# Performance work log

Measured on AMD Instinct MI355X. Metric: run time of the kernel, lower is better.

## Reference

```python
import jax, jax.numpy as jnp
import numpy as np

N_NODES = 100000
N_EDGES = 3200000
DIM = 64


def setup_inputs() -> dict:
    key = jax.random.key(0)
    k1, k2, k3, k4, k5, k6 = jax.random.split(key, 6)
    lap_rows = jax.random.randint(k1, (N_EDGES,), 0, N_NODES, dtype=jnp.int32)
    lap_cols = jax.random.randint(k2, (N_EDGES,), 0, N_NODES, dtype=jnp.int32)
    # normalized-Laplacian-like positive values
    lap_vals = jax.random.uniform(k3, (N_EDGES,), dtype=jnp.float32) * 0.1
    features = jax.random.normal(k4, (N_NODES, DIM), dtype=jnp.float32)
    scale = 1.0 / np.sqrt(DIM)
    W1 = jax.random.normal(k5, (DIM, DIM), dtype=jnp.float32) * scale
    b1 = jnp.zeros((DIM,), dtype=jnp.float32)
    W2 = jax.random.normal(k6, (DIM, DIM), dtype=jnp.float32) * scale
    b2 = jnp.zeros((DIM,), dtype=jnp.float32)
    return {
        "lap_rows": lap_rows, "lap_cols": lap_cols, "lap_vals": lap_vals,
        "features": features, "W1": W1, "b1": b1, "W2": W2, "b2": b2,
    }


def reference(lap_rows, lap_cols, lap_vals, features, W1, b1, W2, b2):
    # x = L @ features  (COO SpMM: gather source rows, scale, scatter-add to dest)
    msgs = lap_vals[:, None] * features[lap_cols]            # [E, D]
    x = jax.ops.segment_sum(msgs, lap_rows, num_segments=N_NODES)  # [N, D]
    # output = (L+I) E W1 + (L E * E) W2
    inter_part1 = (features + x) @ W1 + b1                   # [N, D_out]
    inter_part2 = (x * features) @ W2 + b2                   # [N, D_out]
    return inter_part1 + inter_part2
```

## Files before the change

### kernel.cpp

```cpp
#include <hip/hip_runtime.h>
#include <hip/hip_fp16.h>

#define DIM 64
#define RPB 64
#define RPB_SHIFT 6
#define CAP 6144
#define CAPK (CAP / 1024)
#define HTILE 16384

typedef _Float16 half8 __attribute__((ext_vector_type(8)));
typedef float    f32x4 __attribute__((ext_vector_type(4)));

__global__ __launch_bounds__(256) void scatter_kernel(
    const int* __restrict__ rows, const int* __restrict__ cols,
    const float* __restrict__ vals, const float* __restrict__ feat,
    float* __restrict__ x, int E)
{
    unsigned long long t = (unsigned long long)blockIdx.x * blockDim.x + threadIdx.x;
    int e = (int)(t >> 6);
    int d = (int)(t & 63);
    if (e >= E) return;
    int r = rows[e];
    int c = cols[e];
    float v = vals[e];
    float f = feat[(size_t)c * DIM + d];
    atomicAdd(&x[(size_t)r * DIM + d], v * f);
}

__global__ __launch_bounds__(256) void cvt_kernel(
    const float* __restrict__ f, __half* __restrict__ h, int n2)
{
    int i = blockIdx.x * blockDim.x + threadIdx.x;
    if (i < n2) {
        float2 v = ((const float2*)f)[i];
        __half2 o;
        o.x = __float2half(v.x);
        o.y = __float2half(v.y);
        ((__half2*)h)[i] = o;
    }
}

__global__ __launch_bounds__(1024) void hist_kernel(
    const int* __restrict__ rows, int* __restrict__ gcnt, int E, int B)
{
    extern __shared__ int lcnt[];
    for (int i = threadIdx.x; i < B; i += 1024) lcnt[i] = 0;
    __syncthreads();
    int base = blockIdx.x * HTILE;
#pragma unroll
    for (int k = 0; k < HTILE / 1024; ++k) {
        int e = base + k * 1024 + threadIdx.x;
        if (e < E) atomicAdd(&lcnt[rows[e] >> RPB_SHIFT], 1);
    }
    __syncthreads();
    for (int i = threadIdx.x; i < B; i += 1024)
        if (lcnt[i]) atomicAdd(&gcnt[i], lcnt[i]);
}

__global__ __launch_bounds__(1024) void scan_kernel(
    const int* __restrict__ gcnt, int* __restrict__ offs,
    int* __restrict__ cursors, int B, int E)
{
    __shared__ int lds[2048];
    int t = threadIdx.x;
    int c0 = (t < B) ? gcnt[t] : 0;
    int c1 = (t + 1024 < B) ? gcnt[t + 1024] : 0;
    lds[t] = c0;
    lds[t + 1024] = c1;
    __syncthreads();
    for (int off = 1; off < 2048; off <<= 1) {
        int a = (t >= off) ? lds[t - off] : 0;
        int b = lds[t + 1024 - off];
        __syncthreads();
        lds[t] += a;
        lds[t + 1024] += b;
        __syncthreads();
    }
    if (t < B)        { offs[t] = lds[t] - c0;               cursors[t] = lds[t] - c0; }
    if (t + 1024 < B) { offs[t + 1024] = lds[t + 1024] - c1; cursors[t + 1024] = lds[t + 1024] - c1; }
    if (t == 0) offs[B] = E;
}

__global__ __launch_bounds__(1024) void binpack_kernel(
    const int* __restrict__ rows, const int* __restrict__ cols,
    const float* __restrict__ vals, int* __restrict__ cursors,
    unsigned long long* __restrict__ sorted, int E, int B)
{
    extern __shared__ int l[];
    int* cnt = l;
    int* bse = l + B;
    for (int i = threadIdx.x; i < B; i += 1024) cnt[i] = 0;
    __syncthreads();
    int tbase = blockIdx.x * HTILE;
#pragma unroll
    for (int k = 0; k < HTILE / 1024; ++k) {
        int e = tbase + k * 1024 + threadIdx.x;
        if (e < E) atomicAdd(&cnt[rows[e] >> RPB_SHIFT], 1);
    }
    __syncthreads();
    for (int i = threadIdx.x; i < B; i += 1024) {
        int c = cnt[i];
        bse[i] = c ? atomicAdd(&cursors[i], c) : 0;
    }
    __syncthreads();
    for (int i = threadIdx.x; i < B; i += 1024) cnt[i] = 0;
    __syncthreads();
#pragma unroll
    for (int k = 0; k < HTILE / 1024; ++k) {
        int e = tbase + k * 1024 + threadIdx.x;
        if (e < E) {
            int r = rows[e];
            int b = r >> RPB_SHIFT;
            int slot = bse[b] + atomicAdd(&cnt[b], 1);
            unsigned long long pk =
                ((unsigned long long)__float_as_uint(vals[e]) << 32) |
                ((unsigned long long)(r & (RPB - 1)) << 17) |
                (unsigned)cols[e];
            sorted[slot] = pk;
        }
    }
}

__global__ __launch_bounds__(1024) void reduce_fused_kernel(
    const unsigned long long* __restrict__ sorted, const int* __restrict__ offs,
    const __half* __restrict__ featH, float* __restrict__ x, int N)
{
    __shared__ unsigned long long spk[CAP];
    __shared__ int rcnt[RPB];
    __shared__ int rbase[RPB];

    const int tid = threadIdx.x;
    const int b   = blockIdx.x;
    const int s    = offs[b];
    const int tend = offs[b + 1];
    int nl = tend - s;
    if (nl > CAP) nl = CAP;

    if (tid < RPB) rcnt[tid] = 0;
    __syncthreads();

    unsigned long long pkreg[CAPK];
#pragma unroll
    for (int k = 0; k < CAPK; ++k) {
        int i = k * 1024 + tid;
        pkreg[k] = (i < nl) ? sorted[s + i] : 0ull;
    }
#pragma unroll
    for (int k = 0; k < CAPK; ++k) {
        int i = k * 1024 + tid;
        if (i < nl) atomicAdd(&rcnt[(int)((pkreg[k] >> 17) & (RPB - 1))], 1);
    }
    __syncthreads();

    if (tid < 64) {
        int c = rcnt[tid];
        int v = c;
#pragma unroll
        for (int off = 1; off < 64; off <<= 1) {
            int u = __shfl_up(v, off, 64);
            if (tid >= off) v += u;
        }
        rbase[tid] = v - c;
        rcnt[tid]  = 0;
    }
    __syncthreads();

#pragma unroll
    for (int k = 0; k < CAPK; ++k) {
        int i = k * 1024 + tid;
        if (i < nl) {
            int rl  = (int)((pkreg[k] >> 17) & (RPB - 1));
            int idx = atomicAdd(&rcnt[rl], 1);
            spk[rbase[rl] + idx] = pkreg[k];
        }
    }
    __syncthreads();

    const int w    = tid >> 6;
    const int lane = tid & 63;
    const int eg   = lane >> 3;
    const int sub  = lane & 7;
    const int rowbase = b * RPB;

#pragma unroll
    for (int j = 0; j < RPB / 16; ++j) {
        int rl = w + 16 * j;
        int rs = rbase[rl];
        int rt = rs + rcnt[rl];

        __half2 hacc[4];
#pragma unroll
        for (int q = 0; q < 4; ++q) hacc[q] = __floats2half2_rn(0.f, 0.f);

        int i = rs + eg;
        for (; i + 24 < rt; i += 32) {
            unsigned long long pk0 = spk[i];
            unsigned long long pk1 = spk[i + 8];
            unsigned long long pk2 = spk[i + 16];
            unsigned long long pk3 = spk[i + 24];
            float4 rw0 = *(const float4*)(featH + (size_t)(pk0 & 0x1FFFFu) * DIM + sub * 8);
            float4 rw1 = *(const float4*)(featH + (size_t)(pk1 & 0x1FFFFu) * DIM + sub * 8);
            float4 rw2 = *(const float4*)(featH + (size_t)(pk2 & 0x1FFFFu) * DIM + sub * 8);
            float4 rw3 = *(const float4*)(featH + (size_t)(pk3 & 0x1FFFFu) * DIM + sub * 8);
            __half2 v0 = __float2half2_rn(__uint_as_float((unsigned)(pk0 >> 32)));
            __half2 v1 = __float2half2_rn(__uint_as_float((unsigned)(pk1 >> 32)));
            __half2 v2 = __float2half2_rn(__uint_as_float((unsigned)(pk2 >> 32)));
            __half2 v3 = __float2half2_rn(__uint_as_float((unsigned)(pk3 >> 32)));
            hacc[0] = __hfma2(v0, __builtin_bit_cast(__half2, rw0.x), hacc[0]);
            hacc[1] = __hfma2(v0, __builtin_bit_cast(__half2, rw0.y), hacc[1]);
            hacc[2] = __hfma2(v0, __builtin_bit_cast(__half2, rw0.z), hacc[2]);
            hacc[3] = __hfma2(v0, __builtin_bit_cast(__half2, rw0.w), hacc[3]);
            hacc[0] = __hfma2(v1, __builtin_bit_cast(__half2, rw1.x), hacc[0]);
            hacc[1] = __hfma2(v1, __builtin_bit_cast(__half2, rw1.y), hacc[1]);
            hacc[2] = __hfma2(v1, __builtin_bit_cast(__half2, rw1.z), hacc[2]);
            hacc[3] = __hfma2(v1, __builtin_bit_cast(__half2, rw1.w), hacc[3]);
            hacc[0] = __hfma2(v2, __builtin_bit_cast(__half2, rw2.x), hacc[0]);
            hacc[1] = __hfma2(v2, __builtin_bit_cast(__half2, rw2.y), hacc[1]);
            hacc[2] = __hfma2(v2, __builtin_bit_cast(__half2, rw2.z), hacc[2]);
            hacc[3] = __hfma2(v2, __builtin_bit_cast(__half2, rw2.w), hacc[3]);
            hacc[0] = __hfma2(v3, __builtin_bit_cast(__half2, rw3.x), hacc[0]);
            hacc[1] = __hfma2(v3, __builtin_bit_cast(__half2, rw3.y), hacc[1]);
            hacc[2] = __hfma2(v3, __builtin_bit_cast(__half2, rw3.z), hacc[2]);
            hacc[3] = __hfma2(v3, __builtin_bit_cast(__half2, rw3.w), hacc[3]);
        }
        for (; i < rt; i += 8) {
            unsigned long long pk0 = spk[i];
            float4 rw0 = *(const float4*)(featH + (size_t)(pk0 & 0x1FFFFu) * DIM + sub * 8);
            __half2 v0 = __float2half2_rn(__uint_as_float((unsigned)(pk0 >> 32)));
            hacc[0] = __hfma2(v0, __builtin_bit_cast(__half2, rw0.x), hacc[0]);
            hacc[1] = __hfma2(v0, __builtin_bit_cast(__half2, rw0.y), hacc[1]);
            hacc[2] = __hfma2(v0, __builtin_bit_cast(__half2, rw0.z), hacc[2]);
            hacc[3] = __hfma2(v0, __builtin_bit_cast(__half2, rw0.w), hacc[3]);
        }

        float acc[8];
#pragma unroll
        for (int q = 0; q < 4; ++q) {
            acc[2 * q]     = __low2float(hacc[q]);
            acc[2 * q + 1] = __high2float(hacc[q]);
        }
#pragma unroll
        for (int off = 8; off < 64; off <<= 1) {
#pragma unroll
            for (int q = 0; q < 8; ++q)
                acc[q] += __shfl_xor(acc[q], off, 64);
        }

        int gr = rowbase + rl;
        if (gr < N) {
            if (eg == 0) {
                float4 o; o.x = acc[0]; o.y = acc[1]; o.z = acc[2]; o.w = acc[3];
                *(float4*)(x + (size_t)gr * DIM + sub * 8) = o;
            } else if (eg == 1) {
                float4 o; o.x = acc[4]; o.y = acc[5]; o.z = acc[6]; o.w = acc[7];
                *(float4*)(x + (size_t)gr * DIM + sub * 8 + 4) = o;
            }
        }
    }

    if (tend - s > CAP) {
        __syncthreads();
        for (int e = s + CAP + tid; e < tend; e += 1024) {
            unsigned long long pk = sorted[e];
            int rl = (int)((pk >> 17) & (RPB - 1));
            float v = __uint_as_float((unsigned)(pk >> 32));
            int c = (int)(pk & 0x1FFFFu);
            int gr = rowbase + rl;
            if (gr < N)
                for (int d = 0; d < DIM; ++d)
                    atomicAdd(&x[(size_t)gr * DIM + d],
                              v * __half2float(featH[(size_t)c * DIM + d]));
        }
    }
}

__global__ __launch_bounds__(256) void transform_mfma_kernel(
    const __half* __restrict__ featH, const float* __restrict__ x,
    const float* __restrict__ W1, const float* __restrict__ b1,
    const float* __restrict__ W2, const float* __restrict__ b2,
    float* __restrict__ out, int N)
{
    const int lane = threadIdx.x & 63;
    const int m    = lane & 15;
    const int quad = lane >> 4;

    half8 wfrag[4][4];
#pragma unroll
    for (int t = 0; t < 4; ++t) {
        const float* Wsrc = (t < 2) ? W1 : W2;
        int kbase = (t & 1) * 32 + quad * 8;
#pragma unroll
        for (int c = 0; c < 4; ++c) {
            int col = c * 16 + m;
            half8 w;
#pragma unroll
            for (int j = 0; j < 8; ++j)
                w[j] = (_Float16)Wsrc[(kbase + j) * DIM + col];
            wfrag[t][c] = w;
        }
    }
    float bias[4];
#pragma unroll
    for (int c = 0; c < 4; ++c)
        bias[c] = b1[c * 16 + m] + b2[c * 16 + m];

    const int ntiles = (N + 15) / 16;
    const int wid    = (int)((blockIdx.x * blockDim.x + threadIdx.x) >> 6);
    const int nwaves = (int)((gridDim.x * blockDim.x) >> 6);

    for (int tile = wid; tile < ntiles; tile += nwaves) {
        int row  = tile * 16 + m;
        int rldr = (row < N) ? row : (N - 1);
        const __half* fp = featH + (size_t)rldr * DIM + quad * 8;
        const float*  xp = x     + (size_t)rldr * DIM + quad * 8;
        half8 flo = *(const half8*)(fp);
        half8 fhi = *(const half8*)(fp + 32);
        float4 xl0 = *(const float4*)(xp);
        float4 xl1 = *(const float4*)(xp + 4);
        float4 xh0 = *(const float4*)(xp + 32);
        float4 xh1 = *(const float4*)(xp + 36);

        half8 alo, ahi, blo, bhi;
        _Float16 xv;
        xv = (_Float16)xl0.x; alo[0] = flo[0] + xv; blo[0] = flo[0] * xv;
        xv = (_Float16)xl0.y; alo[1] = flo[1] + xv; blo[1] = flo[1] * xv;
        xv = (_Float16)xl0.z; alo[2] = flo[2] + xv; blo[2] = flo[2] * xv;
        xv = (_Float16)xl0.w; alo[3] = flo[3] + xv; blo[3] = flo[3] * xv;
        xv = (_Float16)xl1.x; alo[4] = flo[4] + xv; blo[4] = flo[4] * xv;
        xv = (_Float16)xl1.y; alo[5] = flo[5] + xv; blo[5] = flo[5] * xv;
        xv = (_Float16)xl1.z; alo[6] = flo[6] + xv; blo[6] = flo[6] * xv;
        xv = (_Float16)xl1.w; alo[7] = flo[7] + xv; blo[7] = flo[7] * xv;
        xv = (_Float16)xh0.x; ahi[0] = fhi[0] + xv; bhi[0] = fhi[0] * xv;
        xv = (_Float16)xh0.y; ahi[1] = fhi[1] + xv; bhi[1] = fhi[1] * xv;
        xv = (_Float16)xh0.z; ahi[2] = fhi[2] + xv; bhi[2] = fhi[2] * xv;
        xv = (_Float16)xh0.w; ahi[3] = fhi[3] + xv; bhi[3] = fhi[3] * xv;
        xv = (_Float16)xh1.x; ahi[4] = fhi[4] + xv; bhi[4] = fhi[4] * xv;
        xv = (_Float16)xh1.y; ahi[5] = fhi[5] + xv; bhi[5] = fhi[5] * xv;
        xv = (_Float16)xh1.z; ahi[6] = fhi[6] + xv; bhi[6] = fhi[6] * xv;
        xv = (_Float16)xh1.w; ahi[7] = fhi[7] + xv; bhi[7] = fhi[7] * xv;

        f32x4 acc[4];
#pragma unroll
        for (int c = 0; c < 4; ++c) {
            f32x4 a0 = { bias[c], bias[c], bias[c], bias[c] };
            a0 = __builtin_amdgcn_mfma_f32_16x16x32_f16(alo, wfrag[0][c], a0, 0, 0, 0);
            a0 = __builtin_amdgcn_mfma_f32_16x16x32_f16(ahi, wfrag[1][c], a0, 0, 0, 0);
            a0 = __builtin_amdgcn_mfma_f32_16x16x32_f16(blo, wfrag[2][c], a0, 0, 0, 0);
            a0 = __builtin_amdgcn_mfma_f32_16x16x32_f16(bhi, wfrag[3][c], a0, 0, 0, 0);
            acc[c] = a0;
        }

#pragma unroll
        for (int reg = 0; reg < 4; ++reg) {
            int orow = tile * 16 + quad * 4 + reg;
            if (orow < N) {
#pragma unroll
                for (int c = 0; c < 4; ++c)
                    out[(size_t)orow * DIM + c * 16 + m] = acc[c][reg];
            }
        }
    }
}

extern "C" void kernel_launch(void* const* d_in, const int* in_sizes, int n_in,
                              void* d_out, int out_size, void* d_ws, size_t ws_size,
                              hipStream_t stream)
{
    const int*   rows = (const int*)d_in[0];
    const int*   cols = (const int*)d_in[1];
    const float* vals = (const float*)d_in[2];
    const float* feat = (const float*)d_in[3];
    const float* W1   = (const float*)d_in[4];
    const float* b1   = (const float*)d_in[5];
    const float* W2   = (const float*)d_in[6];
    const float* b2   = (const float*)d_in[7];
    float* out = (float*)d_out;

    const int E = in_sizes[0];
    const int N = in_sizes[3] / DIM;
    const int B = (N + RPB - 1) / RPB;

    char* ws = (char*)d_ws;
    size_t xBytes     = (size_t)N * DIM * sizeof(float);
    size_t hBytes     = (((size_t)N * DIM * sizeof(__half)) + 255) / 256 * 256;
    size_t offsBytes  = (((size_t)(B + 1) * sizeof(int)) + 255) / 256 * 256;
    size_t cursBytes  = (((size_t)B * sizeof(int)) + 255) / 256 * 256;
    size_t sortBytes  = (size_t)E * 8;

    float*              x       = (float*)ws;
    __half*             featH   = (__half*)(ws + xBytes);
    int*                offs    = (int*)(ws + xBytes + hBytes);
    int*                cursors = (int*)(ws + xBytes + hBytes + offsBytes);
    unsigned long long* sorted  = (unsigned long long*)(ws + xBytes + hBytes + offsBytes + cursBytes);
    size_t need = xBytes + hBytes + offsBytes + cursBytes + sortBytes;

    const int NT = (E + HTILE - 1) / HTILE;

    cvt_kernel<<<(N * DIM / 2 + 255) / 256, 256, 0, stream>>>(feat, featH, N * DIM / 2);

    if (ws_size >= need && B <= 2048 && N <= 131072) {
        hipMemsetAsync(offs, 0, (size_t)(B + 1) * sizeof(int), stream);
        hist_kernel<<<NT, 1024, (size_t)B * 4, stream>>>(rows, offs, E, B);
        scan_kernel<<<1, 1024, 0, stream>>>(offs, offs, cursors, B, E);
        binpack_kernel<<<NT, 1024, (size_t)B * 8, stream>>>(rows, cols, vals,
                                                            cursors, sorted, E, B);
        reduce_fused_kernel<<<B, 1024, 0, stream>>>(sorted, offs, featH, x, N);
    } else {
        hipMemsetAsync(x, 0, xBytes, stream);
        unsigned long long threads = (unsigned long long)E * DIM;
        unsigned int blocks = (unsigned int)((threads + 255ull) / 256ull);
        scatter_kernel<<<blocks, 256, 0, stream>>>(rows, cols, vals, feat, x, E);
    }

    transform_mfma_kernel<<<640, 256, 0, stream>>>(featH, x, W1, b1, W2, b2, out, N);
}
```

Before: 273.9 us.

## Split single-pass edge binning into coarse superbin and fine bin passes

Replaces the one-pass bucket scatter of edges into 64-row bins with two passes. The first pass scatters into 64 superbins of 2048 rows each, and the second re-scatters each superbin into its 32 fine bins, locating the superbin with a binary search over its offsets. The aim is scattered writes that land in far fewer destinations per tile, which improves write locality and reduces cursor atomic contention. In exchange, the packed edge array is read and written a second time, and workspace doubles.

```diff
diff --git a/kernel.cpp b/kernel.cpp
--- a/kernel.cpp
+++ b/kernel.cpp
@@ -4,9 +4,13 @@
 #define DIM 64
 #define RPB 64
 #define RPB_SHIFT 6
+#define SUP_SHIFT 11
+#define SB_MAX 64
 #define CAP 6144
 #define CAPK (CAP / 1024)
-#define HTILE 16384
+#define HTILE_H 16384
+#define HTILE1 8192
+#define HTILE2 4096
 
 typedef _Float16 half8 __attribute__((ext_vector_type(8)));
 typedef float    f32x4 __attribute__((ext_vector_type(4)));
@@ -46,9 +50,9 @@
     extern __shared__ int lcnt[];
     for (int i = threadIdx.x; i < B; i += 1024) lcnt[i] = 0;
     __syncthreads();
-    int base = blockIdx.x * HTILE;
-#pragma unroll
-    for (int k = 0; k < HTILE / 1024; ++k) {
+    int base = blockIdx.x * HTILE_H;
+#pragma unroll
+    for (int k = 0; k < HTILE_H / 1024; ++k) {
         int e = base + k * 1024 + threadIdx.x;
         if (e < E) atomicAdd(&lcnt[rows[e] >> RPB_SHIFT], 1);
     }
@@ -58,8 +62,8 @@
 }
 
 __global__ __launch_bounds__(1024) void scan_kernel(
-    const int* __restrict__ gcnt, int* __restrict__ offs,
-    int* __restrict__ cursors, int B, int E)
+    const int* __restrict__ gcnt, int* __restrict__ offs, int* __restrict__ cursors,
+    int* __restrict__ soffs, int* __restrict__ scursors, int B, int SB, int E)
 {
     __shared__ int lds[2048];
     int t = threadIdx.x;
@@ -76,47 +80,106 @@
         lds[t + 1024] += b;
         __syncthreads();
     }
-    if (t < B)        { offs[t] = lds[t] - c0;               cursors[t] = lds[t] - c0; }
-    if (t + 1024 < B) { offs[t + 1024] = lds[t + 1024] - c1; cursors[t + 1024] = lds[t + 1024] - c1; }
-    if (t == 0) offs[B] = E;
-}
-
-__global__ __launch_bounds__(1024) void binpack_kernel(
+    if (t < B) {
+        int e = lds[t] - c0;
+        offs[t] = e; cursors[t] = e;
+        if ((t & 31) == 0) { soffs[t >> 5] = e; scursors[t >> 5] = e; }
+    }
+    int t2 = t + 1024;
+    if (t2 < B) {
+        int e = lds[t2] - c1;
+        offs[t2] = e; cursors[t2] = e;
+        if ((t2 & 31) == 0) { soffs[t2 >> 5] = e; scursors[t2 >> 5] = e; }
+    }
+    if (t == 0) { offs[B] = E; soffs[SB] = E; }
+}
+
+__global__ __launch_bounds__(1024) void superbin_kernel(
     const int* __restrict__ rows, const int* __restrict__ cols,
-    const float* __restrict__ vals, int* __restrict__ cursors,
-    unsigned long long* __restrict__ sorted, int E, int B)
+    const float* __restrict__ vals, int* __restrict__ scursors,
+    unsigned long long* __restrict__ sorted1, int E, int SB)
+{
+    __shared__ int cnt[SB_MAX];
+    __shared__ int bse[SB_MAX];
+    const int tid = threadIdx.x;
+    if (tid < SB) cnt[tid] = 0;
+    __syncthreads();
+    const int tbase = blockIdx.x * HTILE1;
+    int rr[HTILE1 / 1024];
+#pragma unroll
+    for (int k = 0; k < HTILE1 / 1024; ++k) {
+        int e = tbase + k * 1024 + tid;
+        rr[k] = (e < E) ? rows[e] : -1;
+        if (rr[k] >= 0) atomicAdd(&cnt[rr[k] >> SUP_SHIFT], 1);
+    }
+    __syncthreads();
+    if (tid < SB) {
+        int c = cnt[tid];
+        bse[tid] = c ? atomicAdd(&scursors[tid], c) : 0;
+        cnt[tid] = 0;
+    }
+    __syncthreads();
+#pragma unroll
+    for (int k = 0; k < HTILE1 / 1024; ++k) {
+        int e = tbase + k * 1024 + tid;
+        if (rr[k] >= 0) {
+            int r  = rr[k];
+            int sb = r >> SUP_SHIFT;
+            int slot = bse[sb] + atomicAdd(&cnt[sb], 1);
+            unsigned long long pk =
+                ((unsigned long long)__float_as_uint(vals[e]) << 32) |
+                ((unsigned long long)(r & 2047) << 17) |
+                (unsigned)cols[e];
+            sorted1[slot] = pk;
+        }
+    }
+}
+
+__global__ __launch_bounds__(1024) void finebin_kernel(
+    const unsigned long long* __restrict__ sorted1, const int* __restrict__ soffs,
+    int* __restrict__ cursors, unsigned long long* __restrict__ sorted2,
+    int E, int B, int SB)
 {
     extern __shared__ int l[];
-    int* cnt = l;
-    int* bse = l + B;
-    for (int i = threadIdx.x; i < B; i += 1024) cnt[i] = 0;
-    __syncthreads();
-    int tbase = blockIdx.x * HTILE;
-#pragma unroll
-    for (int k = 0; k < HTILE / 1024; ++k) {
-        int e = tbase + k * 1024 + threadIdx.x;
-        if (e < E) atomicAdd(&cnt[rows[e] >> RPB_SHIFT], 1);
-    }
-    __syncthreads();
-    for (int i = threadIdx.x; i < B; i += 1024) {
+    int* cnt  = l;
+    int* bse  = l + B;
+    int* sofl = l + 2 * B;
+    const int tid = threadIdx.x;
+    if (tid <= SB) sofl[tid] = soffs[tid];
+    for (int i = tid; i < B; i += 1024) cnt[i] = 0;
+    __syncthreads();
+
+    const int tbase = blockIdx.x * HTILE2;
+    unsigned long long pkr[HTILE2 / 1024];
+    int fidr[HTILE2 / 1024];
+#pragma unroll
+    for (int k = 0; k < HTILE2 / 1024; ++k) {
+        int i = tbase + k * 1024 + tid;
+        if (i < E) {
+            pkr[k] = sorted1[i];
+            int lo = 0, hi = SB - 1;
+            while (lo < hi) {
+                int mid = (lo + hi + 1) >> 1;
+                if (sofl[mid] <= i) lo = mid; else hi = mid - 1;
+            }
+            fidr[k] = (lo << 5) + (int)((pkr[k] >> 23) & 31);
+            atomicAdd(&cnt[fidr[k]], 1);
+        } else fidr[k] = -1;
+    }
+    __syncthreads();
+    for (int i = tid; i < B; i += 1024) {
         int c = cnt[i];
         bse[i] = c ? atomicAdd(&cursors[i], c) : 0;
     }
     __syncthreads();
-    for (int i = threadIdx.x; i < B; i += 1024) cnt[i] = 0;
-    __syncthreads();
-#pragma unroll
-    for (int k = 0; k < HTILE / 1024; ++k) {
-        int e = tbase + k * 1024 + threadIdx.x;
-        if (e < E) {
-            int r = rows[e];
-            int b = r >> RPB_SHIFT;
-            int slot = bse[b] + atomicAdd(&cnt[b], 1);
-            unsigned long long pk =
-                ((unsigned long long)__float_as_uint(vals[e]) << 32) |
-                ((unsigned long long)(r & (RPB - 1)) << 17) |
-                (unsigned)cols[e];
-            sorted[slot] = pk;
+    for (int i = tid; i < B; i += 1024) cnt[i] = 0;
+    __syncthreads();
+#pragma unroll
+    for (int k = 0; k < HTILE2 / 1024; ++k) {
+        if (fidr[k] >= 0) {
+            int f = fidr[k];
+            int slot = bse[f] + atomicAdd(&cnt[f], 1);
+            sorted2[slot] = pkr[k];
         }
     }
 }
@@ -376,35 +439,44 @@
     const float* b2   = (const float*)d_in[7];
     float* out = (float*)d_out;
 
-    const int E = in_sizes[0];
-    const int N = in_sizes[3] / DIM;
-    const int B = (N + RPB - 1) / RPB;
+    const int E  = in_sizes[0];
+    const int N  = in_sizes[3] / DIM;
+    const int B  = (N + RPB - 1) / RPB;
+    const int SB = (B + 31) / 32;
 
     char* ws = (char*)d_ws;
     size_t xBytes     = (size_t)N * DIM * sizeof(float);
     size_t hBytes     = (((size_t)N * DIM * sizeof(__half)) + 255) / 256 * 256;
     size_t offsBytes  = (((size_t)(B + 1) * sizeof(int)) + 255) / 256 * 256;
     size_t cursBytes  = (((size_t)B * sizeof(int)) + 255) / 256 * 256;
+    size_t soffBytes  = (((size_t)(SB + 1) * sizeof(int)) + 255) / 256 * 256;
+    size_t scurBytes  = (((size_t)SB * sizeof(int)) + 255) / 256 * 256;
     size_t sortBytes  = (size_t)E * 8;
 
-    float*              x       = (float*)ws;
-    __half*             featH   = (__half*)(ws + xBytes);
-    int*                offs    = (int*)(ws + xBytes + hBytes);
-    int*                cursors = (int*)(ws + xBytes + hBytes + offsBytes);
-    unsigned long long* sorted  = (unsigned long long*)(ws + xBytes + hBytes + offsBytes + cursBytes);
-    size_t need = xBytes + hBytes + offsBytes + cursBytes + sortBytes;
-
-    const int NT = (E + HTILE - 1) / HTILE;
+    float*              x        = (float*)ws;
+    __half*             featH    = (__half*)(ws + xBytes);
+    int*                offs     = (int*)(ws + xBytes + hBytes);
+    int*                cursors  = (int*)(ws + xBytes + hBytes + offsBytes);
+    int*                soffs    = (int*)(ws + xBytes + hBytes + offsBytes + cursBytes);
+    int*                scursors = (int*)(ws + xBytes + hBytes + offsBytes + cursBytes + soffBytes);
+    unsigned long long* sorted1  = (unsigned long long*)(ws + xBytes + hBytes + offsBytes +
+                                                         cursBytes + soffBytes + scurBytes);
+    unsigned long long* sorted2  = sorted1 + E;
+    size_t need = xBytes + hBytes + offsBytes + cursBytes + soffBytes + scurBytes + 2 * sortBytes;
 
     cvt_kernel<<<(N * DIM / 2 + 255) / 256, 256, 0, stream>>>(feat, featH, N * DIM / 2);
 
-    if (ws_size >= need && B <= 2048 && N <= 131072) {
+    if (ws_size >= need && B <= 2048 && SB <= SB_MAX && N <= 131072) {
+        const int NTH = (E + HTILE_H - 1) / HTILE_H;
+        const int NT1 = (E + HTILE1 - 1) / HTILE1;
+        const int NT2 = (E + HTILE2 - 1) / HTILE2;
         hipMemsetAsync(offs, 0, (size_t)(B + 1) * sizeof(int), stream);
-        hist_kernel<<<NT, 1024, (size_t)B * 4, stream>>>(rows, offs, E, B);
-        scan_kernel<<<1, 1024, 0, stream>>>(offs, offs, cursors, B, E);
-        binpack_kernel<<<NT, 1024, (size_t)B * 8, stream>>>(rows, cols, vals,
-                                                            cursors, sorted, E, B);
-        reduce_fused_kernel<<<B, 1024, 0, stream>>>(sorted, offs, featH, x, N);
+        hist_kernel<<<NTH, 1024, (size_t)B * 4, stream>>>(rows, offs, E, B);
+        scan_kernel<<<1, 1024, 0, stream>>>(offs, offs, cursors, soffs, scursors, B, SB, E);
+        superbin_kernel<<<NT1, 1024, 0, stream>>>(rows, cols, vals, scursors, sorted1, E, SB);
+        finebin_kernel<<<NT2, 1024, (size_t)(2 * B + SB + 1) * 4, stream>>>(
+            sorted1, soffs, cursors, sorted2, E, B, SB);
+        reduce_fused_kernel<<<B, 1024, 0, stream>>>(sorted2, offs, featH, x, N);
     } else {
         hipMemsetAsync(x, 0, xBytes, stream);
         unsigned long long threads = (unsigned long long)E * DIM;
```

New measurement: 252.1 us. 1.09x faster.
